# Kernel tuning notes

Measured on AMD Instinct MI355X. Metric: run time of the kernel, lower is better.

The kernel has to match this reference:

```python
import math
import jax, jax.numpy as jnp
import numpy as np

EPS = 1e-6

def rmsnorm(x, g):
    # RMSNorm: x / rms(x) * g
    return x * jax.lax.rsqrt(jnp.mean(x * x, axis=-1, keepdims=True) + EPS) * g

def setup_inputs() -> dict:
    key = jax.random.key(0)
    ks = jax.random.split(key, 10)
    B, S, D, H = 1, 4096, 1024, 16
    dh = D // H
    s = 0.02  # init scale for weights
    x = jax.random.normal(ks[0], (B, S, D), dtype=jnp.float32)
    # causal mask: masked_fill(mask == 0, -inf) => lower-triangular ones
    mask = jnp.tril(jnp.ones((S, S), dtype=jnp.int32))
    WQ = jax.random.normal(ks[1], (H, D, dh), dtype=jnp.float32) * s
    WK = jax.random.normal(ks[2], (H, D, dh), dtype=jnp.float32) * s
    WV = jax.random.normal(ks[3], (H, D, dh), dtype=jnp.float32) * s
    WO = jax.random.normal(ks[4], (D, D), dtype=jnp.float32) * s
    W1 = jax.random.normal(ks[5], (D, 4 * D), dtype=jnp.float32) * s
    B1 = jnp.zeros((4 * D,), dtype=jnp.float32)
    W2 = jax.random.normal(ks[6], (4 * D, D), dtype=jnp.float32) * s
    B2 = jnp.zeros((D,), dtype=jnp.float32)
    g1 = jnp.ones((D,), dtype=jnp.float32)
    g2 = jnp.ones((D,), dtype=jnp.float32)
    return {"x": x, "mask": mask, "g1": g1, "WQ": WQ, "WK": WK, "WV": WV,
            "WO": WO, "g2": g2, "W1": W1, "B1": B1, "W2": W2, "B2": B2}

def reference(x, mask, g1, WQ, WK, WV, WO, g2, W1, B1, W2, B2):
    dh = WQ.shape[-1]
    # --- attention sub-block (pre-norm) ---
    h = rmsnorm(x, g1)                                   # [B,S,D]
    Q = jnp.einsum('bsd,hde->bhse', h, WQ)               # [B,H,S,dh]
    K = jnp.einsum('bsd,hde->bhse', h, WK)
    V = jnp.einsum('bsd,hde->bhse', h, WV)
    # rope() in the source is identity
    scores = jnp.einsum('bhse,bhte->bhst', Q, K) / math.sqrt(dh)  # [B,H,S,S]
    scores = jnp.where(mask == 0, -jnp.inf, scores)
    attn = jax.nn.softmax(scores, axis=-1)
    o = jnp.einsum('bhst,bhte->bhse', attn, V)           # [B,H,S,dh]
    Bn, H, S, e = o.shape
    o = o.transpose(0, 2, 1, 3).reshape(Bn, S, H * e)    # concat heads on last dim
    x = x + o @ WO
    # --- MLP sub-block (pre-norm) ---
    h2 = rmsnorm(x, g2)
    m = jax.nn.relu(h2 @ W1 + B1) @ W2 + B2
    return x + m
```

## Files before the change

### kernel.cpp

```cpp
#include <hip/hip_runtime.h>
#include <hip/hip_bf16.h>

typedef __attribute__((ext_vector_type(8))) short bf16x8;
typedef __attribute__((ext_vector_type(4))) float f32x4;
typedef __attribute__((ext_vector_type(4))) short s16x4;

#define GLOBAL_AS(p) ((const __attribute__((address_space(1))) void*)(p))
#define LDS_AS(p)    ((__attribute__((address_space(3))) void*)(p))

__device__ __forceinline__ short f2bf(float f) {
  return __builtin_bit_cast(short, __float2bfloat16(f));
}
__device__ __forceinline__ float bf2f(short s) {
  return __bfloat162float(__builtin_bit_cast(__hip_bfloat16, s));
}

__global__ __launch_bounds__(256) void pack_qkv_kernel(
    const float* __restrict__ WQ, const float* __restrict__ WK,
    const float* __restrict__ WV, short* __restrict__ out) {
  __shared__ short Ls[64][66];
  const int tid = threadIdx.x;
  const int l = tid & 63, q4 = tid >> 6;
  const int hh = blockIdx.y & 15, proj = blockIdx.y >> 4;
  const float* W = (proj == 0) ? WQ : ((proj == 1) ? WK : WV);
  const float scl = (proj == 0) ? 0.125f : 1.f;
  const int d0 = blockIdx.x * 64;
#pragma unroll
  for (int rep = 0; rep < 16; ++rep) {
    int dd = q4 * 16 + rep;
    Ls[dd][l] = f2bf(W[(size_t)hh * 65536 + (size_t)(d0 + dd) * 64 + l] * scl);
  }
  __syncthreads();
#pragma unroll
  for (int rep = 0; rep < 16; ++rep) {
    int ee = q4 * 16 + rep;
    out[(size_t)(proj * 1024 + hh * 64 + ee) * 1024 + d0 + l] = Ls[l][ee];
  }
}

__global__ __launch_bounds__(256) void transpose_bf16_kernel(
    const float* __restrict__ in, short* __restrict__ out, int R, int C) {
  __shared__ short Ls[64][66];
  const int tid = threadIdx.x;
  const int l = tid & 63, q4 = tid >> 6;
  const int c0 = blockIdx.x * 64, r0 = blockIdx.y * 64;
#pragma unroll
  for (int rep = 0; rep < 16; ++rep) {
    int rr = q4 * 16 + rep;
    Ls[rr][l] = f2bf(in[(size_t)(r0 + rr) * C + c0 + l]);
  }
  __syncthreads();
#pragma unroll
  for (int rep = 0; rep < 16; ++rep) {
    int cc = q4 * 16 + rep;
    out[(size_t)(c0 + cc) * R + r0 + l] = Ls[l][cc];
  }
}

__global__ __launch_bounds__(256) void rmsnorm_kernel(
    const float* __restrict__ x, const float* __restrict__ g,
    short* __restrict__ out, int D) {
  const int row = blockIdx.x;
  const int tid = threadIdx.x;
  const float4 xv = *(const float4*)&x[(size_t)row * D + tid * 4];
  float ss = xv.x * xv.x + xv.y * xv.y + xv.z * xv.z + xv.w * xv.w;
#pragma unroll
  for (int off = 32; off; off >>= 1) ss += __shfl_xor(ss, off);
  __shared__ float red[4];
  if ((tid & 63) == 0) red[tid >> 6] = ss;
  __syncthreads();
  float tot = red[0] + red[1] + red[2] + red[3];
  float scale = rsqrtf(tot / (float)D + 1e-6f);
  const float4 gv = *(const float4*)&g[tid * 4];
  s16x4 o;
  o[0] = f2bf(xv.x * scale * gv.x);
  o[1] = f2bf(xv.y * scale * gv.y);
  o[2] = f2bf(xv.z * scale * gv.z);
  o[3] = f2bf(xv.w * scale * gv.w);
  *(s16x4*)&out[(size_t)row * D + tid * 4] = o;
}

template <int EPI>
__global__ __launch_bounds__(256) void gemm_bt_kernel(
    const short* __restrict__ A, const short* __restrict__ BT,
    int M, int N, int K,
    short* __restrict__ outB, float* __restrict__ outF,
    const float* __restrict__ bias, const float* __restrict__ addend) {
  __shared__ short As[128 * 32];
  __shared__ short Bs[128 * 32];
  const int tid = threadIdx.x;
  const int lane = tid & 63;
  const int wid = tid >> 6;
  const int lrow = lane & 15;
  const int kk = lane >> 4;
  const int row0 = blockIdx.y * 128;
  const int col0 = blockIdx.x * 128;
  const int wm = wid >> 1, wn = wid & 1;

  f32x4 acc[4][4] = {};

  for (int k0 = 0; k0 < K; k0 += 32) {
    __syncthreads();
#pragma unroll
    for (int it = 0; it < 2; ++it) {
      int c = it * 256 + tid;
      int r = c >> 2, c8 = (c & 3) * 8;
      const short* ga = A + (size_t)(row0 + r) * K + k0 + c8;
      const short* gb = BT + (size_t)(col0 + r) * K + k0 + c8;
      short* la = &As[(size_t)(it * 256 + wid * 64) * 8];
      short* lb = &Bs[(size_t)(it * 256 + wid * 64) * 8];
      __builtin_amdgcn_global_load_lds(GLOBAL_AS(ga), LDS_AS(la), 16, 0, 0);
      __builtin_amdgcn_global_load_lds(GLOBAL_AS(gb), LDS_AS(lb), 16, 0, 0);
    }
    __syncthreads();

    bf16x8 a[4], b[4];
#pragma unroll
    for (int i = 0; i < 4; ++i)
      a[i] = *(const bf16x8*)&As[(wm * 64 + i * 16 + lrow) * 32 + kk * 8];
#pragma unroll
    for (int i = 0; i < 4; ++i)
      b[i] = *(const bf16x8*)&Bs[(wn * 64 + i * 16 + lrow) * 32 + kk * 8];
#pragma unroll
    for (int i = 0; i < 4; ++i)
#pragma unroll
      for (int j = 0; j < 4; ++j)
        acc[i][j] = __builtin_amdgcn_mfma_f32_16x16x32_bf16(a[i], b[j], acc[i][j], 0, 0, 0);
  }

#pragma unroll
  for (int i = 0; i < 4; ++i) {
    int row = row0 + wm * 64 + i * 16 + kk * 4;
#pragma unroll
    for (int j = 0; j < 4; ++j) {
      int col = col0 + wn * 64 + j * 16 + lrow;
#pragma unroll
      for (int r = 0; r < 4; ++r) {
        float v = acc[i][j][r];
        size_t o = (size_t)(row + r) * N + col;
        if (EPI == 0) {
          outB[o] = f2bf(v);
        } else if (EPI == 1) {
          outF[o] = v + addend[o];
        } else if (EPI == 2) {
          v += bias[col];
          outB[o] = f2bf(v > 0.f ? v : 0.f);
        } else {
          outF[o] = v + bias[col] + addend[o];
        }
      }
    }
  }
}

#define READ_A(buf, mh)                                                      \
  _Pragma("unroll") for (int m4 = 0; m4 < 4; ++m4) {                         \
    int row_ = wm * 128 + ((mh)*4 + m4) * 16 + lrow;                         \
    _Pragma("unroll") for (int k_ = 0; k_ < 2; ++k_) {                       \
      int sl_ = (k_ * 4 + kk) ^ (row_ & 7);                                  \
      aA[m4][k_] = *(const bf16x8*)&lds[buf][0][row_ * 64 + sl_ * 8];        \
    }                                                                        \
  }
#define READ_B2(buf, pr)                                                     \
  _Pragma("unroll") for (int nn = 0; nn < 2; ++nn) {                         \
    int n_ = (pr)*2 + nn;                                                    \
    int row_ = wn * 64 + n_ * 16 + lrow;                                     \
    _Pragma("unroll") for (int k_ = 0; k_ < 2; ++k_) {                       \
      int sl_ = (k_ * 4 + kk) ^ (row_ & 7);                                  \
      bB[n_][k_] = *(const bf16x8*)&lds[buf][1][row_ * 64 + sl_ * 8];        \
    }                                                                        \
  }
#define MFMA16(mh, nh)                                                       \
  _Pragma("unroll") for (int m4 = 0; m4 < 4; ++m4)                           \
  _Pragma("unroll") for (int n2 = 0; n2 < 2; ++n2)                           \
  _Pragma("unroll") for (int k_ = 0; k_ < 2; ++k_)                           \
    acc[(mh)*4 + m4][(nh)*2 + n2] = __builtin_amdgcn_mfma_f32_16x16x32_bf16( \
        aA[m4][k_], bB[(nh)*2 + n2][k_], acc[(mh)*4 + m4][(nh)*2 + n2], 0, 0, 0);
#define STAGE_HALF(buf, mat, half, kt)                                       \
  {                                                                          \
    const short* g_ = ((mat) ? Bb : Ab) + (size_t)((half)*128) * K + (kt)*64;\
    short* l_ = &lds[buf][mat][(half)*8192];                                 \
    _Pragma("unroll") for (int it_ = 0; it_ < 2; ++it_) {                    \
      int ci_ = it_ * 512 + tid;                                             \
      int r_ = ci_ >> 3, sl_ = (ci_ & 7) ^ (r_ & 7);                         \
      __builtin_amdgcn_global_load_lds(GLOBAL_AS(g_ + (size_t)r_ * K + sl_ * 8), \
                                       LDS_AS(l_ + ci_ * 8), 16, 0, 0);      \
    }                                                                        \
  }
#define PH_SYNC1()                                                           \
  __builtin_amdgcn_s_barrier();                                              \
  asm volatile("s_waitcnt lgkmcnt(0)" ::: "memory");                         \
  __builtin_amdgcn_sched_barrier(0);                                         \
  __builtin_amdgcn_s_setprio(1)
#define PH_SYNC2()                                                           \
  __builtin_amdgcn_s_setprio(0);                                             \
  __builtin_amdgcn_s_barrier()
#define PH_SYNC2_VM(n)                                                       \
  __builtin_amdgcn_s_setprio(0);                                             \
  asm volatile("s_waitcnt vmcnt(" #n ")" ::: "memory");                      \
  __builtin_amdgcn_s_barrier()

template <int EPI>
__global__ __launch_bounds__(512, 2) void gemm256_kernel(
    const short* __restrict__ A, const short* __restrict__ BT,
    int N, int K, int kslice, size_t pstride,
    short* __restrict__ outB, const float* __restrict__ bias) {
  __shared__ short lds[2][2][16384];
  const int tid = threadIdx.x;
  const int lane = tid & 63, wid = tid >> 6;
  const int lrow = lane & 15, kk = lane >> 4;
  const int wm = wid >> 2, wn = wid & 3;
  const int row0 = blockIdx.y * 256, col0 = blockIdx.x * 256;
  const int kbase = blockIdx.z * kslice;
  const int NT = kslice >> 6;

  const short* Ab = A + (size_t)row0 * K + kbase;
  const short* Bb = BT + (size_t)col0 * K + kbase;

  f32x4 acc[8][4] = {};
  bf16x8 aA[4][2], bB[4][2];

  STAGE_HALF(0, 1, 0, 0); STAGE_HALF(0, 0, 0, 0);
  STAGE_HALF(0, 1, 1, 0); STAGE_HALF(0, 0, 1, 0);
  STAGE_HALF(1, 1, 0, 1); STAGE_HALF(1, 0, 0, 1); STAGE_HALF(1, 0, 1, 1);
  asm volatile("s_waitcnt vmcnt(6)" ::: "memory");
  __builtin_amdgcn_s_barrier();

  const int iters = NT >> 1;
  for (int i = 0; i < iters; ++i) {
    const int t1 = 2 * i + 1;
    int kt2 = 2 * i + 2; if (kt2 >= NT) kt2 -= NT;
    int kt3 = 2 * i + 3; if (kt3 >= NT) kt3 -= NT;
    READ_A(0, 0); READ_B2(0, 0); STAGE_HALF(1, 1, 1, t1);
    PH_SYNC1(); MFMA16(0, 0); PH_SYNC2();
    READ_B2(0, 1);
    PH_SYNC1(); MFMA16(0, 1); PH_SYNC2();
    READ_A(0, 1); STAGE_HALF(0, 1, 0, kt2);
    PH_SYNC1(); MFMA16(1, 0); PH_SYNC2();
    STAGE_HALF(0, 0, 0, kt2);
    PH_SYNC1(); MFMA16(1, 1); PH_SYNC2_VM(4);
    READ_A(1, 0); READ_B2(1, 0); STAGE_HALF(0, 1, 1, kt2);
    PH_SYNC1(); MFMA16(0, 0); PH_SYNC2();
    READ_B2(1, 1); STAGE_HALF(0, 0, 1, kt2);
    PH_SYNC1(); MFMA16(0, 1); PH_SYNC2();
    READ_A(1, 1); STAGE_HALF(1, 1, 0, kt3);
    PH_SYNC1(); MFMA16(1, 0); PH_SYNC2();
    STAGE_HALF(1, 0, 0, kt3); STAGE_HALF(1, 0, 1, kt3);
    PH_SYNC1(); MFMA16(1, 1); PH_SYNC2_VM(6);
  }

  short* ob = outB + (size_t)blockIdx.z * pstride;
#pragma unroll
  for (int m = 0; m < 8; ++m) {
    int row = row0 + wm * 128 + m * 16 + kk * 4;
#pragma unroll
    for (int n = 0; n < 4; ++n) {
      int col = col0 + wn * 64 + n * 16 + lrow;
#pragma unroll
      for (int r = 0; r < 4; ++r) {
        float v = acc[m][n][r];
        size_t o = (size_t)(row + r) * N + col;
        if (EPI == 0) {
          ob[o] = f2bf(v);
        } else {
          v += bias[col];
          ob[o] = f2bf(v > 0.f ? v : 0.f);
        }
      }
    }
  }
}

__global__ __launch_bounds__(256) void reduce4_kernel(
    const short* __restrict__ part, const float* __restrict__ bias,
    const float* __restrict__ addend, float* __restrict__ out) {
  const size_t MN = (size_t)4096 * 1024;
  size_t i8 = ((size_t)blockIdx.x * 256 + threadIdx.x) * 8;
  bf16x8 p0 = *(const bf16x8*)&part[i8];
  bf16x8 p1 = *(const bf16x8*)&part[MN + i8];
  bf16x8 p2 = *(const bf16x8*)&part[2 * MN + i8];
  bf16x8 p3 = *(const bf16x8*)&part[3 * MN + i8];
  int col = (int)(i8 & 1023);
#pragma unroll
  for (int j = 0; j < 8; ++j) {
    float v = (bf2f(p0[j]) + bf2f(p1[j])) + (bf2f(p2[j]) + bf2f(p3[j]));
    out[i8 + j] = v + bias[col + j] + addend[i8 + j];
  }
}

__device__ const unsigned char QT_SLOT[48] = {
    31, 31, 30, 15, 30, 29, 29, 28, 14, 28, 27, 27, 26, 13, 26, 25,
    25, 24, 12, 24, 23, 23, 22, 11, 22, 21, 21, 20, 10, 20, 19, 19,
    18,  9, 18, 17, 17, 16,  8, 16,  7,  6,  5,  4,  3,  2,  1,  0};
__device__ const unsigned char SP_SLOT[48] = {
    0, 1, 0, 0, 1, 0, 1, 0, 0, 1, 0, 1, 0, 0, 1, 0,
    1, 0, 0, 1, 0, 1, 0, 0, 1, 0, 1, 0, 0, 1, 0, 1,
    0, 0, 1, 0, 1, 0, 0, 1, 0, 0, 0, 0, 0, 0, 0, 0};

__global__ __launch_bounds__(256) void attn_kernel(
    const short* __restrict__ QK, const short* __restrict__ VT,
    float* __restrict__ opart, float* __restrict__ lpart) {
  const int S = 4096;
  __shared__ short Ks[2][128 * 64];
  __shared__ short Vs[2][64 * 128];
  __shared__ short Ps[4][32 * 64];

  const int tid = threadIdx.x;
  const int lane = tid & 63;
  const int w = tid >> 6;
  const int lrow = lane & 15;
  const int kk = lane >> 4;
  const int bid = blockIdx.x;
  const int h = bid & 15;
  const int slot = bid >> 4;
  const int qtile = QT_SLOT[slot];
  const int sp = SP_SLOT[slot];
  const int T = qtile + 1;
  const bool split = (qtile >= 16);
  const int half = (T + 1) >> 1;
  const int t0 = (split && sp) ? half : 0;
  const int t1 = (split && !sp) ? half : T;
  const int q0 = qtile * 128;
  const int qw = q0 + w * 32;

  auto stage = [&](int buf, int t) {
    const int kv0 = t * 128;
#pragma unroll
    for (int it = 0; it < 4; ++it) {
      int ci = it * 256 + tid;
      int krow = ci >> 3;
      int ksl = (ci & 7) ^ (krow & 7);
      int vrow = ci >> 4;
      int vsl = (ci & 15) ^ (vrow & 15);
      const short* gk = QK + (size_t)(kv0 + krow) * 2048 + 1024 + h * 64 + ksl * 8;
      const short* gv = VT + (size_t)(h * 64 + vrow) * S + kv0 + vsl * 8;
      __builtin_amdgcn_global_load_lds(GLOBAL_AS(gk),
                                       LDS_AS(&Ks[buf][(it * 256 + w * 64) * 8]), 16, 0, 0);
      __builtin_amdgcn_global_load_lds(GLOBAL_AS(gv),
                                       LDS_AS(&Vs[buf][(it * 256 + w * 64) * 8]), 16, 0, 0);
    }
  };

  bf16x8 qf[2][2];
#pragma unroll
  for (int i = 0; i < 2; ++i)
#pragma unroll
    for (int half2 = 0; half2 < 2; ++half2)
      qf[i][half2] = *(const bf16x8*)&QK[(size_t)(qw + i * 16 + lrow) * 2048 +
                                         h * 64 + half2 * 32 + kk * 8];

  float rs_acc[2][4] = {};
  f32x4 o_acc[2][4] = {};

  stage(0, t0);
  __syncthreads();
  int cur = 0;

  for (int t = t0; t < t1; ++t) {
    if (t + 1 < t1) stage(cur ^ 1, t + 1);

#pragma unroll
    for (int h2 = 0; h2 < 2; ++h2) {
      const int kvc = t * 128 + h2 * 64;
      if (kvc > qw + 31) continue;

      bf16x8 kf[4][2];
#pragma unroll
      for (int c = 0; c < 4; ++c)
#pragma unroll
        for (int half2 = 0; half2 < 2; ++half2) {
          int krow = h2 * 64 + c * 16 + lrow;
          kf[c][half2] = *(const bf16x8*)&Ks[cur][krow * 64 + (((half2 * 4 + kk) ^ (lrow & 7)) * 8)];
        }
      f32x4 sc[2][4];
      __builtin_amdgcn_s_setprio(1);
#pragma unroll
      for (int i = 0; i < 2; ++i)
#pragma unroll
        for (int c = 0; c < 4; ++c) {
          f32x4 z = {};
          z = __builtin_amdgcn_mfma_f32_16x16x32_bf16(qf[i][0], kf[c][0], z, 0, 0, 0);
          z = __builtin_amdgcn_mfma_f32_16x16x32_bf16(qf[i][1], kf[c][1], z, 0, 0, 0);
          sc[i][c] = z;
        }
      __builtin_amdgcn_s_setprio(0);

      if (kvc + 63 <= qw) {
#pragma unroll
        for (int i = 0; i < 2; ++i)
#pragma unroll
          for (int r = 0; r < 4; ++r) {
            const int qrow = i * 16 + kk * 4 + r;
            float ps[4];
#pragma unroll
            for (int c = 0; c < 4; ++c) {
              float p = __expf(sc[i][c][r]);
              ps[c] = p;
              int col = c * 16 + lrow;
              Ps[w][qrow * 64 + (((col >> 3) ^ (qrow & 7)) * 8) + (col & 7)] = f2bf(p);
            }
            rs_acc[i][r] += (ps[0] + ps[1]) + (ps[2] + ps[3]);
          }
      } else {
#pragma unroll
        for (int i = 0; i < 2; ++i)
#pragma unroll
          for (int r = 0; r < 4; ++r) {
            const int qrow = i * 16 + kk * 4 + r;
            const int q = qw + qrow;
            float ps[4];
#pragma unroll
            for (int c = 0; c < 4; ++c) {
              float p = __expf(sc[i][c][r]);
              if (kvc + c * 16 + lrow > q) p = 0.f;
              ps[c] = p;
              int col = c * 16 + lrow;
              Ps[w][qrow * 64 + (((col >> 3) ^ (qrow & 7)) * 8) + (col & 7)] = f2bf(p);
            }
            rs_acc[i][r] += (ps[0] + ps[1]) + (ps[2] + ps[3]);
          }
      }

#pragma unroll
      for (int ks = 0; ks < 2; ++ks) {
        bf16x8 pf2[2], vf[4];
#pragma unroll
        for (int i = 0; i < 2; ++i) {
          int qrow = i * 16 + lrow;
          pf2[i] = *(const bf16x8*)&Ps[w][qrow * 64 + (((ks * 4 + kk) ^ (qrow & 7)) * 8)];
        }
#pragma unroll
        for (int g = 0; g < 4; ++g) {
          int erow = g * 16 + lrow;
          vf[g] = *(const bf16x8*)&Vs[cur][erow * 128 + (((h2 * 8 + ks * 4 + kk) ^ (lrow & 15)) * 8)];
        }
        __builtin_amdgcn_s_setprio(1);
#pragma unroll
        for (int i = 0; i < 2; ++i)
#pragma unroll
          for (int g = 0; g < 4; ++g)
            o_acc[i][g] = __builtin_amdgcn_mfma_f32_16x16x32_bf16(pf2[i], vf[g], o_acc[i][g], 0, 0, 0);
        __builtin_amdgcn_s_setprio(0);
      }
    }

    __syncthreads();
    cur ^= 1;
  }

  const int pidx = (h * 32 + qtile) * 2 + sp;
  float* op = opart + (size_t)pidx * 8192;
  float* lp = lpart + pidx * 128;
#pragma unroll
  for (int i = 0; i < 2; ++i)
#pragma unroll
    for (int r = 0; r < 4; ++r) {
      float l = rs_acc[i][r];
      l += __shfl_xor(l, 1);
      l += __shfl_xor(l, 2);
      l += __shfl_xor(l, 4);
      l += __shfl_xor(l, 8);
      if (lrow == 0) lp[w * 32 + i * 16 + kk * 4 + r] = l;
    }
#pragma unroll
  for (int i = 0; i < 2; ++i)
#pragma unroll
    for (int g = 0; g < 4; ++g)
#pragma unroll
      for (int r = 0; r < 4; ++r)
        op[(w * 32 + i * 16 + kk * 4 + r) * 64 + g * 16 + lrow] = o_acc[i][g][r];
}

__global__ __launch_bounds__(256) void attn_combine_kernel(
    const float* __restrict__ opart, const float* __restrict__ lpart,
    short* __restrict__ O) {
  size_t e8 = ((size_t)blockIdx.x * 256 + threadIdx.x) * 8;
  const int srow = (int)(e8 >> 10);
  const int col = (int)(e8 & 1023);
  const int h = col >> 6, d = col & 63;
  const int qtile = srow >> 7, qr = srow & 127;
  const int pb = (h * 32 + qtile) * 2;
  const float* o0 = opart + (size_t)pb * 8192 + qr * 64 + d;
  float l = lpart[pb * 128 + qr];
  float4 a0 = *(const float4*)o0;
  float4 a1 = *(const float4*)(o0 + 4);
  if (qtile >= 16) {
    const float* o1 = opart + (size_t)(pb + 1) * 8192 + qr * 64 + d;
    float4 b0 = *(const float4*)o1;
    float4 b1 = *(const float4*)(o1 + 4);
    a0.x += b0.x; a0.y += b0.y; a0.z += b0.z; a0.w += b0.w;
    a1.x += b1.x; a1.y += b1.y; a1.z += b1.z; a1.w += b1.w;
    l += lpart[(pb + 1) * 128 + qr];
  }
  float inv = 1.f / l;
  bf16x8 o;
  o[0] = f2bf(a0.x * inv); o[1] = f2bf(a0.y * inv);
  o[2] = f2bf(a0.z * inv); o[3] = f2bf(a0.w * inv);
  o[4] = f2bf(a1.x * inv); o[5] = f2bf(a1.y * inv);
  o[6] = f2bf(a1.z * inv); o[7] = f2bf(a1.w * inv);
  *(bf16x8*)&O[e8] = o;
}

extern "C" void kernel_launch(void* const* d_in, const int* in_sizes, int n_in,
                              void* d_out, int out_size, void* d_ws, size_t ws_size,
                              hipStream_t stream) {
  const float* x  = (const float*)d_in[0];
  const float* g1 = (const float*)d_in[2];
  const float* WQ = (const float*)d_in[3];
  const float* WK = (const float*)d_in[4];
  const float* WV = (const float*)d_in[5];
  const float* WO = (const float*)d_in[6];
  const float* g2 = (const float*)d_in[7];
  const float* W1 = (const float*)d_in[8];
  const float* B1 = (const float*)d_in[9];
  const float* W2 = (const float*)d_in[10];
  const float* B2 = (const float*)d_in[11];
  float* out = (float*)d_out;

  const int S = 4096, D = 1024, H = 16;

  char* ws = (char*)d_ws;
  size_t off = 0;
  auto alloc = [&](size_t bytes) -> void* {
    void* p = ws + off;
    off += (bytes + 255) & ~(size_t)255;
    return p;
  };
  short* h1     = (short*)alloc((size_t)S * D * 2);
  short* wqkv_t = (short*)alloc((size_t)3072 * 1024 * 2);
  short* qk     = (short*)alloc((size_t)S * 2048 * 2);
  short* vt     = (short*)alloc((size_t)1024 * S * 2);
  short* attn_o = (short*)alloc((size_t)S * D * 2);
  short* wo_t   = (short*)alloc((size_t)1024 * 1024 * 2);
  float* x2     = (float*)alloc((size_t)S * D * 4);
  short* h2     = (short*)alloc((size_t)S * D * 2);
  short* w1_t   = (short*)alloc((size_t)4096 * 1024 * 2);
  short* m1     = (short*)alloc((size_t)S * 4096 * 2);
  short* w2_t   = (short*)alloc((size_t)1024 * 4096 * 2);
  short* partW2 = qk;
  float* opart  = (float*)m1;
  float* lpart  = (float*)h1;

  pack_qkv_kernel<<<dim3(D / 64, 48), 256, 0, stream>>>(WQ, WK, WV, wqkv_t);
  transpose_bf16_kernel<<<dim3(1024 / 64, 1024 / 64), 256, 0, stream>>>(WO, wo_t, 1024, 1024);
  transpose_bf16_kernel<<<dim3(4096 / 64, 1024 / 64), 256, 0, stream>>>(W1, w1_t, 1024, 4096);
  transpose_bf16_kernel<<<dim3(1024 / 64, 4096 / 64), 256, 0, stream>>>(W2, w2_t, 4096, 1024);

  rmsnorm_kernel<<<S, 256, 0, stream>>>(x, g1, h1, D);
  gemm_bt_kernel<0><<<dim3(2048 / 128, S / 128), 256, 0, stream>>>(
      h1, wqkv_t, S, 2048, 1024, qk, nullptr, nullptr, nullptr);
  gemm_bt_kernel<0><<<dim3(S / 128, 1024 / 128), 256, 0, stream>>>(
      wqkv_t + (size_t)2048 * 1024, h1, 1024, S, 1024, vt, nullptr, nullptr, nullptr);
  attn_kernel<<<dim3(768), 256, 0, stream>>>(qk, vt, opart, lpart);
  attn_combine_kernel<<<dim3((S * 1024 / 8) / 256), 256, 0, stream>>>(opart, lpart, attn_o);
  gemm_bt_kernel<1><<<dim3(1024 / 128, S / 128), 256, 0, stream>>>(
      attn_o, wo_t, S, 1024, 1024, nullptr, x2, nullptr, x);

  rmsnorm_kernel<<<S, 256, 0, stream>>>(x2, g2, h2, D);
  gemm256_kernel<2><<<dim3(4096 / 256, 4096 / 256, 1), 512, 0, stream>>>(
      h2, w1_t, 4096, 1024, 1024, 0, m1, B1);
  gemm256_kernel<0><<<dim3(1024 / 256, 4096 / 256, 4), 512, 0, stream>>>(
      m1, w2_t, 1024, 4096, 1024, (size_t)4096 * 1024, partW2, nullptr);
  reduce4_kernel<<<2048, 256, 0, stream>>>(partW2, B2, x2, out);
}
```

Baseline: 276.8 us.

## Split attention query tile across eight waves of 16 rows each

The attention kernel now runs 512 threads (8 waves) per block instead of 4, with each wave handling 16 query rows rather than 32. The K/V staging loop is halved to match the larger thread count, and the per-wave P buffer shrinks accordingly. The aim is more waves in flight to hide LDS and exp latency and to finer-grain the causal skip. In exchange, each wave reuses every K/V fragment read from LDS for half as many query rows, which doubles LDS traffic per unit of MFMA work.

```diff
diff --git a/kernel.cpp b/kernel.cpp
--- a/kernel.cpp
+++ b/kernel.cpp
@@ -297,13 +297,13 @@
     1, 0, 0, 1, 0, 1, 0, 0, 1, 0, 1, 0, 0, 1, 0, 1,
     0, 0, 1, 0, 1, 0, 0, 1, 0, 0, 0, 0, 0, 0, 0, 0};
 
-__global__ __launch_bounds__(256) void attn_kernel(
+__global__ __launch_bounds__(512, 4) void attn_kernel(
     const short* __restrict__ QK, const short* __restrict__ VT,
     float* __restrict__ opart, float* __restrict__ lpart) {
   const int S = 4096;
   __shared__ short Ks[2][128 * 64];
   __shared__ short Vs[2][64 * 128];
-  __shared__ short Ps[4][32 * 64];
+  __shared__ short Ps[8][16 * 64];
 
   const int tid = threadIdx.x;
   const int lane = tid & 63;
@@ -321,13 +321,13 @@
   const int t0 = (split && sp) ? half : 0;
   const int t1 = (split && !sp) ? half : T;
   const int q0 = qtile * 128;
-  const int qw = q0 + w * 32;
+  const int qw = q0 + w * 16;
 
   auto stage = [&](int buf, int t) {
     const int kv0 = t * 128;
 #pragma unroll
-    for (int it = 0; it < 4; ++it) {
-      int ci = it * 256 + tid;
+    for (int it = 0; it < 2; ++it) {
+      int ci = it * 512 + tid;
       int krow = ci >> 3;
       int ksl = (ci & 7) ^ (krow & 7);
       int vrow = ci >> 4;
@@ -335,22 +335,20 @@
       const short* gk = QK + (size_t)(kv0 + krow) * 2048 + 1024 + h * 64 + ksl * 8;
       const short* gv = VT + (size_t)(h * 64 + vrow) * S + kv0 + vsl * 8;
       __builtin_amdgcn_global_load_lds(GLOBAL_AS(gk),
-                                       LDS_AS(&Ks[buf][(it * 256 + w * 64) * 8]), 16, 0, 0);
+                                       LDS_AS(&Ks[buf][(it * 512 + w * 64) * 8]), 16, 0, 0);
       __builtin_amdgcn_global_load_lds(GLOBAL_AS(gv),
-                                       LDS_AS(&Vs[buf][(it * 256 + w * 64) * 8]), 16, 0, 0);
+                                       LDS_AS(&Vs[buf][(it * 512 + w * 64) * 8]), 16, 0, 0);
     }
   };
 
-  bf16x8 qf[2][2];
-#pragma unroll
-  for (int i = 0; i < 2; ++i)
-#pragma unroll
-    for (int half2 = 0; half2 < 2; ++half2)
-      qf[i][half2] = *(const bf16x8*)&QK[(size_t)(qw + i * 16 + lrow) * 2048 +
-                                         h * 64 + half2 * 32 + kk * 8];
-
-  float rs_acc[2][4] = {};
-  f32x4 o_acc[2][4] = {};
+  bf16x8 qf[2];
+#pragma unroll
+  for (int half2 = 0; half2 < 2; ++half2)
+    qf[half2] = *(const bf16x8*)&QK[(size_t)(qw + lrow) * 2048 +
+                                    h * 64 + half2 * 32 + kk * 8];
+
+  float rs_acc[4] = {};
+  f32x4 o_acc[4] = {};
 
   stage(0, t0);
   __syncthreads();
@@ -362,7 +360,7 @@
 #pragma unroll
     for (int h2 = 0; h2 < 2; ++h2) {
       const int kvc = t * 128 + h2 * 64;
-      if (kvc > qw + 31) continue;
+      if (kvc > qw + 15) continue;
 
       bf16x8 kf[4][2];
 #pragma unroll
@@ -372,62 +370,55 @@
           int krow = h2 * 64 + c * 16 + lrow;
           kf[c][half2] = *(const bf16x8*)&Ks[cur][krow * 64 + (((half2 * 4 + kk) ^ (lrow & 7)) * 8)];
         }
-      f32x4 sc[2][4];
+      f32x4 sc[4];
       __builtin_amdgcn_s_setprio(1);
 #pragma unroll
-      for (int i = 0; i < 2; ++i)
-#pragma unroll
-        for (int c = 0; c < 4; ++c) {
-          f32x4 z = {};
-          z = __builtin_amdgcn_mfma_f32_16x16x32_bf16(qf[i][0], kf[c][0], z, 0, 0, 0);
-          z = __builtin_amdgcn_mfma_f32_16x16x32_bf16(qf[i][1], kf[c][1], z, 0, 0, 0);
-          sc[i][c] = z;
-        }
+      for (int c = 0; c < 4; ++c) {
+        f32x4 z = {};
+        z = __builtin_amdgcn_mfma_f32_16x16x32_bf16(qf[0], kf[c][0], z, 0, 0, 0);
+        z = __builtin_amdgcn_mfma_f32_16x16x32_bf16(qf[1], kf[c][1], z, 0, 0, 0);
+        sc[c] = z;
+      }
       __builtin_amdgcn_s_setprio(0);
 
       if (kvc + 63 <= qw) {
 #pragma unroll
-        for (int i = 0; i < 2; ++i)
-#pragma unroll
-          for (int r = 0; r < 4; ++r) {
-            const int qrow = i * 16 + kk * 4 + r;
-            float ps[4];
-#pragma unroll
-            for (int c = 0; c < 4; ++c) {
-              float p = __expf(sc[i][c][r]);
-              ps[c] = p;
-              int col = c * 16 + lrow;
-              Ps[w][qrow * 64 + (((col >> 3) ^ (qrow & 7)) * 8) + (col & 7)] = f2bf(p);
-            }
-            rs_acc[i][r] += (ps[0] + ps[1]) + (ps[2] + ps[3]);
+        for (int r = 0; r < 4; ++r) {
+          const int qrow = kk * 4 + r;
+          float ps[4];
+#pragma unroll
+          for (int c = 0; c < 4; ++c) {
+            float p = __expf(sc[c][r]);
+            ps[c] = p;
+            int col = c * 16 + lrow;
+            Ps[w][qrow * 64 + (((col >> 3) ^ (qrow & 7)) * 8) + (col & 7)] = f2bf(p);
           }
+          rs_acc[r] += (ps[0] + ps[1]) + (ps[2] + ps[3]);
+        }
       } else {
 #pragma unroll
-        for (int i = 0; i < 2; ++i)
-#pragma unroll
-          for (int r = 0; r < 4; ++r) {
-            const int qrow = i * 16 + kk * 4 + r;
-            const int q = qw + qrow;
-            float ps[4];
-#pragma unroll
-            for (int c = 0; c < 4; ++c) {
-              float p = __expf(sc[i][c][r]);
-              if (kvc + c * 16 + lrow > q) p = 0.f;
-              ps[c] = p;
-              int col = c * 16 + lrow;
-              Ps[w][qrow * 64 + (((col >> 3) ^ (qrow & 7)) * 8) + (col & 7)] = f2bf(p);
-            }
-            rs_acc[i][r] += (ps[0] + ps[1]) + (ps[2] + ps[3]);
+        for (int r = 0; r < 4; ++r) {
+          const int qrow = kk * 4 + r;
+          const int q = qw + qrow;
+          float ps[4];
+#pragma unroll
+          for (int c = 0; c < 4; ++c) {
+            float p = __expf(sc[c][r]);
+            if (kvc + c * 16 + lrow > q) p = 0.f;
+            ps[c] = p;
+            int col = c * 16 + lrow;
+            Ps[w][qrow * 64 + (((col >> 3) ^ (qrow & 7)) * 8) + (col & 7)] = f2bf(p);
           }
+          rs_acc[r] += (ps[0] + ps[1]) + (ps[2] + ps[3]);
+        }
       }
 
 #pragma unroll
       for (int ks = 0; ks < 2; ++ks) {
-        bf16x8 pf2[2], vf[4];
-#pragma unroll
-        for (int i = 0; i < 2; ++i) {
-          int qrow = i * 16 + lrow;
-          pf2[i] = *(const bf16x8*)&Ps[w][qrow * 64 + (((ks * 4 + kk) ^ (qrow & 7)) * 8)];
+        bf16x8 pf2, vf[4];
+        {
+          int qrow = lrow;
+          pf2 = *(const bf16x8*)&Ps[w][qrow * 64 + (((ks * 4 + kk) ^ (qrow & 7)) * 8)];
         }
 #pragma unroll
         for (int g = 0; g < 4; ++g) {
@@ -436,10 +427,8 @@
         }
         __builtin_amdgcn_s_setprio(1);
 #pragma unroll
-        for (int i = 0; i < 2; ++i)
-#pragma unroll
-          for (int g = 0; g < 4; ++g)
-            o_acc[i][g] = __builtin_amdgcn_mfma_f32_16x16x32_bf16(pf2[i], vf[g], o_acc[i][g], 0, 0, 0);
+        for (int g = 0; g < 4; ++g)
+          o_acc[g] = __builtin_amdgcn_mfma_f32_16x16x32_bf16(pf2, vf[g], o_acc[g], 0, 0, 0);
         __builtin_amdgcn_s_setprio(0);
       }
     }
@@ -452,23 +441,19 @@
   float* op = opart + (size_t)pidx * 8192;
   float* lp = lpart + pidx * 128;
 #pragma unroll
-  for (int i = 0; i < 2; ++i)
-#pragma unroll
-    for (int r = 0; r < 4; ++r) {
-      float l = rs_acc[i][r];
-      l += __shfl_xor(l, 1);
-      l += __shfl_xor(l, 2);
-      l += __shfl_xor(l, 4);
-      l += __shfl_xor(l, 8);
-      if (lrow == 0) lp[w * 32 + i * 16 + kk * 4 + r] = l;
-    }
-#pragma unroll
-  for (int i = 0; i < 2; ++i)
-#pragma unroll
-    for (int g = 0; g < 4; ++g)
-#pragma unroll
-      for (int r = 0; r < 4; ++r)
-        op[(w * 32 + i * 16 + kk * 4 + r) * 64 + g * 16 + lrow] = o_acc[i][g][r];
+  for (int r = 0; r < 4; ++r) {
+    float l = rs_acc[r];
+    l += __shfl_xor(l, 1);
+    l += __shfl_xor(l, 2);
+    l += __shfl_xor(l, 4);
+    l += __shfl_xor(l, 8);
+    if (lrow == 0) lp[w * 16 + kk * 4 + r] = l;
+  }
+#pragma unroll
+  for (int g = 0; g < 4; ++g)
+#pragma unroll
+    for (int r = 0; r < 4; ++r)
+      op[(w * 16 + kk * 4 + r) * 64 + g * 16 + lrow] = o_acc[g][r];
 }
 
 __global__ __launch_bounds__(256) void attn_combine_kernel(
@@ -551,7 +536,7 @@
       h1, wqkv_t, S, 2048, 1024, qk, nullptr, nullptr, nullptr);
   gemm_bt_kernel<0><<<dim3(S / 128, 1024 / 128), 256, 0, stream>>>(
       wqkv_t + (size_t)2048 * 1024, h1, 1024, S, 1024, vt, nullptr, nullptr, nullptr);
-  attn_kernel<<<dim3(768), 256, 0, stream>>>(qk, vt, opart, lpart);
+  attn_kernel<<<dim3(768), 512, 0, stream>>>(qk, vt, opart, lpart);
   attn_combine_kernel<<<dim3((S * 1024 / 8) / 256), 256, 0, stream>>>(opart, lpart, attn_o);
   gemm_bt_kernel<1><<<dim3(1024 / 128, S / 128), 256, 0, stream>>>(
       attn_o, wo_t, S, 1024, 1024, nullptr, x2, nullptr, x);
```

New measurement: 266.3 us. 1.04x faster.
